# Optimization experiments

Measured on AMD Instinct MI355X. Metric: run time of the kernel, lower is better.

The kernel has to match this reference:

```python
import jax, jax.numpy as jnp
import numpy as np

B, N, D, H = 8, 1024, 256, 8
HD = D // H  # head_dim = 32
EPS = 1e-06


def setup_inputs() -> dict:
    key = jax.random.key(0)
    ks = jax.random.split(key, 8)
    x = jax.random.normal(ks[0], (B, N, D), dtype=jnp.float32)
    adj = jax.random.randint(ks[1], (B, N, N), 0, 2, dtype=jnp.int32)
    # Parameters
    W_w = jax.random.normal(ks[2], (D, D), dtype=jnp.float32) / np.sqrt(D)
    W_b = jnp.zeros((D,), dtype=jnp.float32)
    # a: xavier_uniform over [num_heads, 2*head_dim]
    lim = np.sqrt(6.0 / (H + 2 * HD))
    a = jax.random.uniform(ks[3], (H, 2 * HD), minval=-lim, maxval=lim, dtype=jnp.float32)
    gamma = jnp.ones((D,), dtype=jnp.float32)
    beta = jnp.zeros((D,), dtype=jnp.float32)
    return {"x": x, "adj": adj, "W_w": W_w, "W_b": W_b, "a": a, "gamma": gamma, "beta": beta}


def reference(x, adj, W_w, W_b, a, gamma, beta):
    residual = x
    h = jnp.einsum('bnd,od->bno', x, W_w) + W_b          # [B,N,D]
    h = h.reshape(B, N, H, HD).transpose(0, 2, 1, 3)     # [B,H,N,hd]
    # Faithful to original einsum 'bnijh,bh->bnij': `a` is indexed by the
    # BATCH axis (requires batch==num_heads). Decompose concat-dot into two
    # O(N) projections summed pairwise (same math, no O(N^2) concat tensor).
    s_i = jnp.einsum('bhnd,bd->bhn', h, a[:, :HD])       # [B,H,N]
    s_j = jnp.einsum('bhnd,bd->bhn', h, a[:, HD:])       # [B,H,N]
    scores = s_i[:, :, :, None] + s_j[:, :, None, :]     # [B,H,N,N]
    scores = jnp.where(scores >= 0, scores, 0.2 * scores)  # LeakyReLU(0.2)
    mask = (1.0 - adj.astype(scores.dtype))[:, None] * -1e9
    attn = jax.nn.softmax(scores + mask, axis=-1)        # [B,H,N,N]
    out = jnp.einsum('bhij,bhjd->bhid', attn, h)         # [B,H,N,hd]
    out = out.transpose(0, 2, 1, 3).reshape(B, N, D)
    out = out + residual
    # LayerNorm with torch unbiased std, divide by (std + eps)
    mean = out.mean(axis=-1, keepdims=True)
    var = ((out - mean) ** 2).mean(axis=-1, keepdims=True) * (D / (D - 1))
    out = (out - mean) / (jnp.sqrt(var) + EPS)
    return out * gamma + beta
```

## Files before the change

### kernel.cpp

```cpp
#include <hip/hip_runtime.h>
#include <hip/hip_bf16.h>
#include <math.h>

#define Bq 8
#define Nq 1024
#define Dq 256
#define Hq 8
#define HDq 32
#define LOG2E 1.44269504f

typedef __attribute__((ext_vector_type(8)))  short short8v;
typedef __attribute__((ext_vector_type(4)))  float f32x4;
typedef __attribute__((ext_vector_type(16))) float f32x16;

__device__ __forceinline__ void gload_lds16(const void* g, void* l) {
    __builtin_amdgcn_global_load_lds(
        (const __attribute__((address_space(1))) void*)g,
        (__attribute__((address_space(3))) void*)l, 16, 0, 0);
}

__global__ __launch_bounds__(256) void gemm_pack(const float* __restrict__ x,
                                                 const float* __restrict__ W,
                                                 const float* __restrict__ Wb,
                                                 const float* __restrict__ a,
                                                 const int* __restrict__ adj,
                                                 __hip_bfloat16* __restrict__ h_bT,
                                                 float* __restrict__ s_i2,
                                                 float* __restrict__ s_j2,
                                                 unsigned* __restrict__ adjw) {
    __shared__ __hip_bfloat16 xs[64][68];
    __shared__ __hip_bfloat16 wsm[64][68];
    __shared__ __hip_bfloat16 ht[64][72];
    const int t = threadIdx.x;
    const int lane = t & 63, wv = t >> 6;

    if (blockIdx.x >= 512) {
        const size_t row = ((size_t)blockIdx.x - 512) * 4 + wv;
        const int* ar = adj + row * Nq;
        unsigned* wr = adjw + row * 32;
        #pragma unroll
        for (int it = 0; it < 16; ++it) {
            int v = ar[it * 64 + lane];
            unsigned long long mask = __ballot(v != 0);
            if (lane == 0) {
                wr[it * 2 + 0] = (unsigned)mask;
                wr[it * 2 + 1] = (unsigned)(mask >> 32);
            }
        }
        return;
    }

    const int m0 = (blockIdx.x & 127) * 64;
    const int o0 = (blockIdx.x >> 7) * 64;
    const int lo = lane & 31, hi = lane >> 5;
    const int mw = (wv & 1) * 32, ow = (wv >> 1) * 32;
    const int b = m0 >> 10;
    f32x16 acc = 0.f;

    for (int k0 = 0; k0 < 256; k0 += 64) {
        __syncthreads();
        #pragma unroll
        for (int it = 0; it < 4; ++it) {
            int f4  = t + it * 256;
            int row = f4 >> 4;
            int c4  = (f4 & 15) * 4;
            float4 xv = *(const float4*)(x + (size_t)(m0 + row) * 256 + k0 + c4);
            float4 wv2 = *(const float4*)(W + (size_t)(o0 + row) * 256 + k0 + c4);
            union { ushort4 u; __bf16 e[4]; } xb, wb;
            xb.e[0] = (__bf16)xv.x; xb.e[1] = (__bf16)xv.y;
            xb.e[2] = (__bf16)xv.z; xb.e[3] = (__bf16)xv.w;
            wb.e[0] = (__bf16)wv2.x; wb.e[1] = (__bf16)wv2.y;
            wb.e[2] = (__bf16)wv2.z; wb.e[3] = (__bf16)wv2.w;
            *(ushort4*)(&xs[row][c4])  = xb.u;
            *(ushort4*)(&wsm[row][c4]) = wb.u;
        }
        __syncthreads();
        #pragma unroll
        for (int kk = 0; kk < 4; ++kk) {
            short8v av = *(const short8v*)(&xs[mw + lo][kk * 16 + hi * 8]);
            short8v bv = *(const short8v*)(&wsm[ow + lo][kk * 16 + hi * 8]);
            acc = __builtin_amdgcn_mfma_f32_32x32x16_bf16(av, bv, acc, 0, 0, 0);
        }
    }

    __syncthreads();
    const float bias = Wb[o0 + ow + lo];
    #pragma unroll
    for (int rg = 0; rg < 16; ++rg) {
        int row = (rg & 3) + 8 * (rg >> 2) + 4 * hi;
        float v = acc[rg] + bias;
        ht[ow + lo][mw + row] = (__hip_bfloat16)v;
    }
    __syncthreads();

    #pragma unroll
    for (int it = 0; it < 2; ++it) {
        int s8 = t + it * 256;
        int ol = s8 >> 3;
        int n8 = (s8 & 7) * 8;
        short8v v = *(const short8v*)(&ht[ol][n8]);
        int o = o0 + ol;
        size_t drow = (size_t)((b * Hq + (o >> 5)) * HDq + (o & 31));
        *(short8v*)((unsigned short*)h_bT + drow * Nq + (m0 & 1023) + n8) = v;
    }
    {
        int which = t >> 7;
        int hd = (t >> 6) & 1, nl = t & 63;
        const float* ab = a + b * 64 + which * 32;
        float s = 0.f;
        #pragma unroll
        for (int d = 0; d < 32; ++d)
            s += (float)ht[hd * 32 + d][nl] * ab[d];
        int bh = b * Hq + (o0 >> 5) + hd;
        int n  = (m0 & 1023) + nl;
        (which ? s_j2 : s_i2)[(size_t)bh * Nq + n] = s * LOG2E;
    }
}

__global__ __launch_bounds__(256, 4) void attn_v8(const __hip_bfloat16* __restrict__ h_bT,
                                                  const unsigned* __restrict__ adjw,
                                                  const float* __restrict__ s_i2,
                                                  const float* __restrict__ s_j2,
                                                  float* __restrict__ att) {
    __shared__ __hip_bfloat16 hsT[32][512];
    __shared__ float sjs[512];
    const int t = threadIdx.x, lane = t & 63, wv = t >> 6;
    const int id = ((int)blockIdx.x & 7) * 128 + ((int)blockIdx.x >> 3);
    const int bh = id >> 4;
    const int b  = bh >> 3, hh = bh & 7;
    const int i0 = (id & 15) * 64 + wv * 16;
    const int r16 = lane & 15, jg = lane >> 4;
    const int iG = i0 + r16;
    const int key = r16 & 7;
    const unsigned shbase = jg * 8;

    const float si = s_i2[(size_t)bh * Nq + iG];
    const unsigned short* hb = (const unsigned short*)h_bT + (size_t)bh * HDq * Nq;
    const float* sjb = s_j2 + (size_t)bh * Nq;
    const unsigned* awp = adjw + ((size_t)b * Nq + iG) * 32;
    const __hip_bfloat16* pr0 = &hsT[r16][0];
    const __hip_bfloat16* pr1 = &hsT[r16 + 16][0];

    short8v ones;
    #pragma unroll
    for (int k = 0; k < 8; ++k) ones[k] = (short)0x3F80;

    f32x4 acc0 = 0.f, acc1 = 0.f, accl = 0.f;

    for (int ch = 0; ch < 2; ++ch) {
        __syncthreads();
        #pragma unroll
        for (int it = 0; it < 8; ++it) {
            int r = wv * 8 + it;
            const unsigned short* src = hb + (size_t)r * Nq + ch * 512
                                      + ((lane ^ (r & 7)) << 3);
            gload_lds16(src, &hsT[r][0]);
        }
        if (wv < 2) {
            const float* s4 = sjb + ch * 512 + wv * 256 + lane * 4;
            gload_lds16(s4, &sjs[wv * 256]);
        }
        __syncthreads();

        uint4 q0 = *(const uint4*)(awp + ch * 16);
        uint4 q1 = *(const uint4*)(awp + ch * 16 + 4);
        uint4 q2 = *(const uint4*)(awp + ch * 16 + 8);
        uint4 q3 = *(const uint4*)(awp + ch * 16 + 12);
        unsigned aw16[16] = {q0.x, q0.y, q0.z, q0.w, q1.x, q1.y, q1.z, q1.w,
                             q2.x, q2.y, q2.z, q2.w, q3.x, q3.y, q3.z, q3.w};

        #pragma unroll
        for (int w = 0; w < 16; ++w) {
            unsigned wbits = aw16[w] >> shbase;
            int po = ((w * 4 + jg) ^ key) << 3;
            short8v fb0 = *(const short8v*)(pr0 + po);
            short8v fb1 = *(const short8v*)(pr1 + po);
            f32x4 sv0 = *(const f32x4*)(&sjs[w * 32 + jg * 8]);
            f32x4 sv1 = *(const f32x4*)(&sjs[w * 32 + jg * 8 + 4]);
            union { short8v v; __bf16 e[8]; } pa;
            #pragma unroll
            for (int e = 0; e < 8; ++e) {
                float sc = si + (e < 4 ? sv0[e] : sv1[e - 4]);
                sc = fmaxf(sc, 0.2f * sc);
                sc = ((wbits >> e) & 1u) ? sc : -30000.f;
                pa.e[e] = (__bf16)__builtin_amdgcn_exp2f(sc);
            }
            acc0 = __builtin_amdgcn_mfma_f32_16x16x32_bf16(pa.v, fb0, acc0, 0, 0, 0);
            acc1 = __builtin_amdgcn_mfma_f32_16x16x32_bf16(pa.v, fb1, acc1, 0, 0, 0);
            accl = __builtin_amdgcn_mfma_f32_16x16x32_bf16(pa.v, ones, accl, 0, 0, 0);
        }
    }

    #pragma unroll
    for (int rg = 0; rg < 4; ++rg) {
        int row = jg * 4 + rg;
        float rl = 1.f / accl[rg];
        size_t base = ((size_t)b * Nq + i0 + row) * Dq + hh * HDq;
        att[base + r16]      = acc0[rg] * rl;
        att[base + 16 + r16] = acc1[rg] * rl;
    }
}

__global__ __launch_bounds__(256) void ln_k(const float* __restrict__ att,
                                            const float* __restrict__ x,
                                            const float* __restrict__ gamma,
                                            const float* __restrict__ beta,
                                            float* __restrict__ out) {
    const int t = threadIdx.x, lane = t & 63, wv = t >> 6;
    const size_t row  = (size_t)blockIdx.x * 4 + wv;
    const size_t base = row * Dq + lane * 4;
    float4 av = *(const float4*)(att + base);
    float4 xv = *(const float4*)(x + base);
    float o0 = av.x + xv.x, o1 = av.y + xv.y;
    float o2 = av.z + xv.z, o3 = av.w + xv.w;
    float s  = o0 + o1 + o2 + o3;
    float sq = o0 * o0 + o1 * o1 + o2 * o2 + o3 * o3;
    #pragma unroll
    for (int off = 32; off; off >>= 1) {
        s  += __shfl_xor(s, off);
        sq += __shfl_xor(sq, off);
    }
    float mean = s * (1.f / 256.f);
    float var  = (sq - 256.f * mean * mean) * (1.f / 255.f);
    var = fmaxf(var, 0.f);
    float inv = 1.f / (sqrtf(var) + 1e-6f);
    float4 g  = *(const float4*)(gamma + lane * 4);
    float4 bt = *(const float4*)(beta + lane * 4);
    float4 ov;
    ov.x = (o0 - mean) * inv * g.x + bt.x;
    ov.y = (o1 - mean) * inv * g.y + bt.y;
    ov.z = (o2 - mean) * inv * g.z + bt.z;
    ov.w = (o3 - mean) * inv * g.w + bt.w;
    *(float4*)(out + base) = ov;
}

extern "C" void kernel_launch(void* const* d_in, const int* in_sizes, int n_in,
                              void* d_out, int out_size, void* d_ws, size_t ws_size,
                              hipStream_t stream) {
    const float* x     = (const float*)d_in[0];
    const int*   adj   = (const int*)d_in[1];
    const float* W_w   = (const float*)d_in[2];
    const float* W_b   = (const float*)d_in[3];
    const float* a     = (const float*)d_in[4];
    const float* gamma = (const float*)d_in[5];
    const float* beta  = (const float*)d_in[6];
    float* out = (float*)d_out;

    __hip_bfloat16* h_bT = (__hip_bfloat16*)d_ws;
    float* att  = (float*)((char*)d_ws + (size_t)Bq * Hq * Nq * HDq * 2);
    float* s_i2 = att + (size_t)Bq * Nq * Dq;
    float* s_j2 = s_i2 + (size_t)Bq * Hq * Nq;
    unsigned* adjw = (unsigned*)(s_j2 + (size_t)Bq * Hq * Nq);

    gemm_pack<<<2560, 256, 0, stream>>>(x, W_w, W_b, a, adj, h_bT, s_i2, s_j2, adjw);
    attn_v8<<<1024, 256, 0, stream>>>(h_bT, adjw, s_i2, s_j2, att);
    ln_k<<<2048, 256, 0, stream>>>(att, x, gamma, beta, out);
}
```

Measured before the change: 45.97 us.

## Double-buffer attention chunks in LDS and store attention output as bf16

The attention kernel now splits the key dimension into four 256-wide chunks and double-buffers the h and s_j tiles in LDS. The next chunk's async global-to-LDS loads are issued before computing the current one, with explicit vmcnt waits and barriers, so load latency overlaps the exp/MFMA work. The intermediate attention output is also written as bf16 instead of fp32, halving that round trip to the LayerNorm kernel. The bf16 intermediate adds rounding error before the residual add and LayerNorm, and the hand-coded waitcnt values depend on the exact number of outstanding loads.

```diff
diff --git a/kernel.cpp b/kernel.cpp
--- a/kernel.cpp
+++ b/kernel.cpp
@@ -117,13 +117,13 @@
     }
 }
 
-__global__ __launch_bounds__(256, 4) void attn_v8(const __hip_bfloat16* __restrict__ h_bT,
+__global__ __launch_bounds__(256, 4) void attn_v9(const __hip_bfloat16* __restrict__ h_bT,
                                                   const unsigned* __restrict__ adjw,
                                                   const float* __restrict__ s_i2,
                                                   const float* __restrict__ s_j2,
-                                                  float* __restrict__ att) {
-    __shared__ __hip_bfloat16 hsT[32][512];
-    __shared__ float sjs[512];
+                                                  __hip_bfloat16* __restrict__ att) {
+    __shared__ __hip_bfloat16 hsT[2][32][256];
+    __shared__ float sjs[2][256];
     const int t = threadIdx.x, lane = t & 63, wv = t >> 6;
     const int id = ((int)blockIdx.x & 7) * 128 + ((int)blockIdx.x >> 3);
     const int bh = id >> 4;
@@ -138,45 +138,56 @@
     const unsigned short* hb = (const unsigned short*)h_bT + (size_t)bh * HDq * Nq;
     const float* sjb = s_j2 + (size_t)bh * Nq;
     const unsigned* awp = adjw + ((size_t)b * Nq + iG) * 32;
-    const __hip_bfloat16* pr0 = &hsT[r16][0];
-    const __hip_bfloat16* pr1 = &hsT[r16 + 16][0];
+
+    auto stage = [&](int nb, int ch) {
+        #pragma unroll
+        for (int it = 0; it < 4; ++it) {
+            int rrb = wv * 8 + it * 2;
+            int rr  = rrb + (lane >> 5);
+            int oct = (lane & 31) ^ (rr & 7);
+            const unsigned short* src = hb + (size_t)rr * Nq + ch * 256 + (oct << 3);
+            gload_lds16(src, &hsT[nb][rrb][0]);
+        }
+        gload_lds16(sjb + ch * 256 + lane * 4, &sjs[nb][0]);
+    };
 
     short8v ones;
     #pragma unroll
     for (int k = 0; k < 8; ++k) ones[k] = (short)0x3F80;
 
     f32x4 acc0 = 0.f, acc1 = 0.f, accl = 0.f;
-
-    for (int ch = 0; ch < 2; ++ch) {
-        __syncthreads();
-        #pragma unroll
-        for (int it = 0; it < 8; ++it) {
-            int r = wv * 8 + it;
-            const unsigned short* src = hb + (size_t)r * Nq + ch * 512
-                                      + ((lane ^ (r & 7)) << 3);
-            gload_lds16(src, &hsT[r][0]);
-        }
-        if (wv < 2) {
-            const float* s4 = sjb + ch * 512 + wv * 256 + lane * 4;
-            gload_lds16(s4, &sjs[wv * 256]);
-        }
-        __syncthreads();
-
-        uint4 q0 = *(const uint4*)(awp + ch * 16);
-        uint4 q1 = *(const uint4*)(awp + ch * 16 + 4);
-        uint4 q2 = *(const uint4*)(awp + ch * 16 + 8);
-        uint4 q3 = *(const uint4*)(awp + ch * 16 + 12);
-        unsigned aw16[16] = {q0.x, q0.y, q0.z, q0.w, q1.x, q1.y, q1.z, q1.w,
-                             q2.x, q2.y, q2.z, q2.w, q3.x, q3.y, q3.z, q3.w};
-
-        #pragma unroll
-        for (int w = 0; w < 16; ++w) {
-            unsigned wbits = aw16[w] >> shbase;
+    uint4 qa[2], qb[2];
+
+    stage(0, 0);
+    qa[0] = *(const uint4*)(awp);
+    qb[0] = *(const uint4*)(awp + 4);
+
+    #pragma unroll
+    for (int c = 0; c < 4; ++c) {
+        const int cb = c & 1;
+        if (c < 3) {
+            stage(cb ^ 1, c + 1);
+            qa[cb ^ 1] = *(const uint4*)(awp + (c + 1) * 8);
+            qb[cb ^ 1] = *(const uint4*)(awp + (c + 1) * 8 + 4);
+        }
+        if (c < 3) asm volatile("s_waitcnt vmcnt(7)" ::: "memory");
+        else       asm volatile("s_waitcnt vmcnt(0)" ::: "memory");
+        __builtin_amdgcn_s_barrier();
+        __builtin_amdgcn_sched_barrier(0);
+
+        unsigned aw8[8] = {qa[cb].x, qa[cb].y, qa[cb].z, qa[cb].w,
+                           qb[cb].x, qb[cb].y, qb[cb].z, qb[cb].w};
+        const __hip_bfloat16* pr0 = &hsT[cb][r16][0];
+        const __hip_bfloat16* pr1 = &hsT[cb][r16 + 16][0];
+
+        #pragma unroll
+        for (int w = 0; w < 8; ++w) {
+            unsigned wbits = aw8[w] >> shbase;
             int po = ((w * 4 + jg) ^ key) << 3;
             short8v fb0 = *(const short8v*)(pr0 + po);
             short8v fb1 = *(const short8v*)(pr1 + po);
-            f32x4 sv0 = *(const f32x4*)(&sjs[w * 32 + jg * 8]);
-            f32x4 sv1 = *(const f32x4*)(&sjs[w * 32 + jg * 8 + 4]);
+            f32x4 sv0 = *(const f32x4*)(&sjs[cb][w * 32 + jg * 8]);
+            f32x4 sv1 = *(const f32x4*)(&sjs[cb][w * 32 + jg * 8 + 4]);
             union { short8v v; __bf16 e[8]; } pa;
             #pragma unroll
             for (int e = 0; e < 8; ++e) {
@@ -189,6 +200,8 @@
             acc1 = __builtin_amdgcn_mfma_f32_16x16x32_bf16(pa.v, fb1, acc1, 0, 0, 0);
             accl = __builtin_amdgcn_mfma_f32_16x16x32_bf16(pa.v, ones, accl, 0, 0, 0);
         }
+        asm volatile("s_waitcnt lgkmcnt(0)" ::: "memory");
+        __builtin_amdgcn_s_barrier();
     }
 
     #pragma unroll
@@ -196,12 +209,12 @@
         int row = jg * 4 + rg;
         float rl = 1.f / accl[rg];
         size_t base = ((size_t)b * Nq + i0 + row) * Dq + hh * HDq;
-        att[base + r16]      = acc0[rg] * rl;
-        att[base + 16 + r16] = acc1[rg] * rl;
-    }
-}
-
-__global__ __launch_bounds__(256) void ln_k(const float* __restrict__ att,
+        att[base + r16]      = (__hip_bfloat16)(acc0[rg] * rl);
+        att[base + 16 + r16] = (__hip_bfloat16)(acc1[rg] * rl);
+    }
+}
+
+__global__ __launch_bounds__(256) void ln_k(const __hip_bfloat16* __restrict__ att,
                                             const float* __restrict__ x,
                                             const float* __restrict__ gamma,
                                             const float* __restrict__ beta,
@@ -209,10 +222,11 @@
     const int t = threadIdx.x, lane = t & 63, wv = t >> 6;
     const size_t row  = (size_t)blockIdx.x * 4 + wv;
     const size_t base = row * Dq + lane * 4;
-    float4 av = *(const float4*)(att + base);
+    union { ushort4 u; __hip_bfloat16 e[4]; } av;
+    av.u = *(const ushort4*)((const unsigned short*)att + base);
     float4 xv = *(const float4*)(x + base);
-    float o0 = av.x + xv.x, o1 = av.y + xv.y;
-    float o2 = av.z + xv.z, o3 = av.w + xv.w;
+    float o0 = (float)av.e[0] + xv.x, o1 = (float)av.e[1] + xv.y;
+    float o2 = (float)av.e[2] + xv.z, o3 = (float)av.e[3] + xv.w;
     float s  = o0 + o1 + o2 + o3;
     float sq = o0 * o0 + o1 * o1 + o2 * o2 + o3 * o3;
     #pragma unroll
@@ -247,12 +261,12 @@
     float* out = (float*)d_out;
 
     __hip_bfloat16* h_bT = (__hip_bfloat16*)d_ws;
-    float* att  = (float*)((char*)d_ws + (size_t)Bq * Hq * Nq * HDq * 2);
-    float* s_i2 = att + (size_t)Bq * Nq * Dq;
+    __hip_bfloat16* att  = (__hip_bfloat16*)((char*)d_ws + (size_t)Bq * Hq * Nq * HDq * 2);
+    float* s_i2 = (float*)((char*)att + (size_t)Bq * Nq * Dq * 2);
     float* s_j2 = s_i2 + (size_t)Bq * Hq * Nq;
     unsigned* adjw = (unsigned*)(s_j2 + (size_t)Bq * Hq * Nq);
 
     gemm_pack<<<2560, 256, 0, stream>>>(x, W_w, W_b, a, adj, h_bT, s_i2, s_j2, adjw);
-    attn_v8<<<1024, 256, 0, stream>>>(h_bT, adjw, s_i2, s_j2, att);
+    attn_v9<<<1024, 256, 0, stream>>>(h_bT, adjw, s_i2, s_j2, att);
     ln_k<<<2048, 256, 0, stream>>>(att, x, gamma, beta, out);
 }
```

New measurement: 45.08 us. Within noise of the previous version (-1.9%).
